# Kernel optimization log

Hardware: AMD Instinct MI355X
Metric: run time of the kernel (lower is better)

The kernel has to match this reference:

```python
import jax, jax.numpy as jnp
import numpy as np


def _ln(x, w, b, eps=1e-5):
    m = x.mean(-1, keepdims=True)
    v = jnp.mean((x - m) ** 2, axis=-1, keepdims=True)
    return (x - m) * jax.lax.rsqrt(v + eps) * w + b


def _to_seq(xc, g):
    # xc: [B,Di,H,W] -> [B,L,Di]; g0: row-major fwd, g1: row-major rev,
    # g2: col-major fwd, g3: col-major rev (CrossScan_1..4)
    if g >= 2:
        xc = xc.transpose(0, 1, 3, 2)
    s = xc.reshape(xc.shape[0], xc.shape[1], -1)
    if g % 2 == 1:
        s = jnp.flip(s, -1)
    return s.transpose(0, 2, 1)


def _from_seq(y, g, H, W):
    # y: [B,L,Di] -> [B,H,W,Di], inverse of _to_seq (CrossMerge_1..4)
    if g % 2 == 1:
        y = jnp.flip(y, 1)
    Bn, L, Di = y.shape
    if g >= 2:
        return y.reshape(Bn, W, H, Di).transpose(0, 2, 1, 3)
    return y.reshape(Bn, H, W, Di)


def _sscan(dA, dBx, Cm):
    # selective scan: h_t = dA_t*h + dBx_t ; y_t = <h_t, C_t>
    # dA,dBx: [B,L,Di,S], Cm: [B,L,S] -> y: [B,L,Di]
    def step(h, inp):
        a, bx, c = inp
        h = a * h + bx
        return h, jnp.einsum('bds,bs->bd', h, c)
    h0 = jnp.zeros(dA.shape[:1] + dA.shape[2:], dA.dtype)
    _, ys = jax.lax.scan(step, h0, (dA.transpose(1, 0, 2, 3), dBx.transpose(1, 0, 2, 3), Cm.transpose(1, 0, 2)))
    return ys.transpose(1, 0, 2)


def _ss2d(xc, g, H, W, ipw, ipb, cw, cb, xpw, dtw, dtb, A_log, Ds, onw, onb, opw, opb):
    R = dtw.shape[-1]
    S = A_log.shape[-1]
    xz = xc @ ipw.T + ipb                      # [B,H,W,2*Di]
    Di = xz.shape[-1] // 2
    xi, z = xz[..., :Di], xz[..., Di:]
    xi = xi.transpose(0, 3, 1, 2)              # [B,Di,H,W]
    xi = jax.lax.conv_general_dilated(xi, cw, (1, 1), [(1, 1), (1, 1)],
                                      dimension_numbers=('NCHW', 'OIHW', 'NCHW'),
                                      feature_group_count=Di) + cb[None, :, None, None]
    xi = jax.nn.silu(xi)
    seq = _to_seq(xi, g)                       # [B,L,Di]
    xdbl = seq @ xpw.T                         # [B,L,R+2S]
    dtr, Bm, Cm = xdbl[..., :R], xdbl[..., R:R + S], xdbl[..., R + S:]
    dt = jax.nn.softplus(dtr @ dtw.T + dtb)    # [B,L,Di]
    A = -jnp.exp(A_log)                        # [Di,S]
    dA = jnp.exp(dt[..., None] * A)            # [B,L,Di,S]
    dBx = (dt * seq)[..., None] * Bm[:, :, None, :]
    y = _sscan(dA, dBx, Cm) + Ds * seq
    y = _from_seq(y, g, H, W)                  # [B,H,W,Di]
    y = _ln(y, onw, onb)
    y = y * jax.nn.silu(z)
    return y @ opw.T + opb


def setup_inputs() -> dict:
    Bn, Hh, Ww, C = 8, 96, 96, 256
    Di = C // 4
    S = 1
    R = max(1, (Di + 15) // 16)
    key = jax.random.key(0)
    ks = jax.random.split(key, 12)
    nrm = lambda k, sh, s: jax.random.normal(k, sh, jnp.float32) * s
    return {
        'x': nrm(ks[0], (Bn, Hh * Ww, C), 1.0),
        'norm_w': jnp.ones((C,), jnp.float32), 'norm_b': jnp.zeros((C,), jnp.float32),
        'fc_w': nrm(ks[1], (C, C), 0.02), 'fc_b': jnp.zeros((C,), jnp.float32),
        'conv1d_w': nrm(ks[2], (1, 1, 3), 0.3),
        'in_proj_w': nrm(ks[3], (4, 2 * Di, Di), 0.05), 'in_proj_b': jnp.zeros((4, 2 * Di), jnp.float32),
        'conv2d_w': nrm(ks[4], (4, Di, 1, 3, 3), 0.2), 'conv2d_b': jnp.zeros((4, Di), jnp.float32),
        'x_proj_w': nrm(ks[5], (4, R + 2 * S, Di), 0.05),
        'dt_w': nrm(ks[6], (4, Di, R), 0.1), 'dt_b': nrm(ks[7], (4, Di), 0.1),
        'A_log': nrm(ks[8], (4, Di, S), 0.1),
        'Ds': jnp.ones((4, Di), jnp.float32),
        'out_norm_w': jnp.ones((4, Di), jnp.float32), 'out_norm_b': jnp.zeros((4, Di), jnp.float32),
        'out_proj_w': nrm(ks[9], (4, Di, Di), 0.05), 'out_proj_b': jnp.zeros((4, Di), jnp.float32),
        'proj_w': nrm(ks[10], (C, C), 0.02), 'proj_b': jnp.zeros((C,), jnp.float32),
        'skip_scale': jnp.ones((1,), jnp.float32),
        'H': Hh, 'W': Ww,
    }


def reference(x, norm_w, norm_b, fc_w, fc_b, conv1d_w, in_proj_w, in_proj_b, conv2d_w, conv2d_b,
              x_proj_w, dt_w, dt_b, A_log, Ds, out_norm_w, out_norm_b, out_proj_w, out_proj_b,
              proj_w, proj_b, skip_scale, H, W):
    B, N, C = x.shape
    xn = _ln(x, norm_w, norm_b)
    z_avg = xn.mean(1)                         # [B,C] (permute(0,2,1).mean(2))
    yg = jax.lax.conv_general_dilated(z_avg[:, None, :], conv1d_w, (1,), [(1, 1)],
                                      dimension_numbers=('NCH', 'OIH', 'NCH'))[:, 0, :]
    gate = jax.nn.sigmoid(z_avg @ fc_w.T + fc_b + yg)   # fc_out_2 [B,C]
    xg = xn.reshape(B, H, W, C)
    Dg = C // 4
    outs = [_ss2d(xg[..., g * Dg:(g + 1) * Dg], g, H, W,
                  in_proj_w[g], in_proj_b[g], conv2d_w[g], conv2d_b[g], x_proj_w[g],
                  dt_w[g], dt_b[g], A_log[g], Ds[g], out_norm_w[g], out_norm_b[g],
                  out_proj_w[g], out_proj_b[g]) for g in range(4)]
    xm = jnp.concatenate(outs, -1) * skip_scale * xg
    xm = xm.reshape(B, N, C) * gate[:, None, :]
    xm = _ln(xm, norm_w, norm_b)
    return xm @ proj_w.T + proj_b
```

## Files before the change

### kernel.cpp

```cpp
#include <hip/hip_runtime.h>
#include <math.h>

#define HH 96
#define WWI 96
#define NN 9216
#define CC 256
#define LL 9216
#define CHK 96
#define NCH 96
#define BB 8
#define BN (BB*NN)

__device__ __forceinline__ float softplusf(float x){
    float e = expf(-fabsf(x));
    return fmaxf(x, 0.f) + log1pf(e);
}
__device__ __forceinline__ float sigmf(float x){ return 1.f / (1.f + expf(-x)); }

__device__ __forceinline__ float wredsum(float v){
    #pragma unroll
    for(int o = 32; o > 0; o >>= 1) v += __shfl_xor(v, o, 64);
    return v;
}

__device__ __forceinline__ void wredsum2(float& s, float& q){
    #pragma unroll
    for(int o = 32; o > 0; o >>= 1){
        s += __shfl_xor(s, o, 64);
        q += __shfl_xor(q, o, 64);
    }
}

__device__ __forceinline__ void chunk_walk(int g, int chunk, int& base, int& step){
    if(g == 0){ base = chunk * 96;        step = 1;   }
    else if(g == 1){ base = 9215 - chunk * 96; step = -1; }
    else if(g == 2){ base = chunk;        step = 96;  }
    else { base = 9215 - chunk;           step = -96; }
}

__global__ __launch_bounds__(256) void k_stats(const float* __restrict__ x,
                                               float* __restrict__ mrs){
    int wid = threadIdx.x >> 6, lane = threadIdx.x & 63;
    size_t row = (size_t)blockIdx.x * 4 + wid;
    float4 v = ((const float4*)(x + row * CC))[lane];
    float s = wredsum(v.x + v.y + v.z + v.w);
    float q = wredsum(v.x*v.x + v.y*v.y + v.z*v.z + v.w*v.w);
    float m = s * (1.f/256.f);
    float var = q * (1.f/256.f) - m*m;
    float rs = rsqrtf(fmaxf(var, 0.f) + 1e-5f);
    if(lane == 0){ mrs[2*row] = m; mrs[2*row+1] = rs; }
}

__global__ __launch_bounds__(256) void k_stats2(const float* __restrict__ y,
                                                float* __restrict__ mrs2){
    int wid = threadIdx.x >> 6, lane = threadIdx.x & 63;
    size_t row = (size_t)blockIdx.x * 4 + wid;
    size_t b = row / NN, n = row - b * NN;
    int g = lane >> 4, c4 = (lane & 15) * 4;
    float4 v = *(const float4*)(y + (((size_t)b*4 + g)*NN + n)*64 + c4);
    float s = wredsum(v.x + v.y + v.z + v.w);
    float q = wredsum(v.x*v.x + v.y*v.y + v.z*v.z + v.w*v.w);
    float m = s * (1.f/256.f);
    float var = q * (1.f/256.f) - m*m;
    float rs = rsqrtf(fmaxf(var, 0.f) + 1e-5f);
    if(lane == 0){ mrs2[2*row] = m; mrs2[2*row+1] = rs; }
}

__global__ __launch_bounds__(256) void k_prew(const float* __restrict__ pw,
        const float* __restrict__ nw, const float* __restrict__ nb,
        const float* __restrict__ pb, float* __restrict__ Wn,
        float* __restrict__ wsum, float* __restrict__ cvec){
    int o = threadIdx.x;
    float ws = 0.f, cc = 0.f;
    for(int k = 0; k < 256; k++){
        float w = pw[(size_t)o * 256 + k];
        float wn = w * nw[k];
        Wn[(size_t)o * 256 + k] = wn;
        ws += wn; cc += w * nb[k];
    }
    wsum[o] = ws; cvec[o] = cc + pb[o];
}

__global__ __launch_bounds__(256) void k_zavg(const float* __restrict__ x,
        const float* __restrict__ mrs, const float* __restrict__ nw,
        const float* __restrict__ nb, float* __restrict__ zpart){
    int c = threadIdx.x, b = blockIdx.y, t0 = blockIdx.x * 256;
    float nwv = nw[c], nbv = nb[c];
    float s = 0.f;
    for(int i = 0; i < 256; i++){
        size_t r = (size_t)b * NN + t0 + i;
        s += (x[r * CC + c] - mrs[2*r]) * mrs[2*r+1] * nwv + nbv;
    }
    zpart[((size_t)b * 36 + blockIdx.x) * CC + c] = s;
}

__global__ __launch_bounds__(256) void k_gate(const float* __restrict__ zpart,
        const float* __restrict__ fcw, const float* __restrict__ fcb,
        const float* __restrict__ w1d, float* __restrict__ gate){
    __shared__ float za[CC];
    int c = threadIdx.x, b = blockIdx.x;
    float s = 0.f;
    for(int t = 0; t < 36; t++) s += zpart[((size_t)b * 36 + t) * CC + c];
    za[c] = s * (1.f/(float)NN);
    __syncthreads();
    float zm1 = (c > 0)     ? za[c-1] : 0.f;
    float zp1 = (c < CC-1)  ? za[c+1] : 0.f;
    float acc = fcb[c] + w1d[0]*zm1 + w1d[1]*za[c] + w1d[2]*zp1;
    const float* wr = fcw + (size_t)c * CC;
    for(int k = 0; k < CC; k++) acc += za[k] * wr[k];
    gate[b * CC + c] = sigmf(acc);
}

template<int ZPRE>
__global__ __launch_bounds__(256) void k_ipconv(const float* __restrict__ x,
        const float* __restrict__ mrs, const float* __restrict__ nw,
        const float* __restrict__ nb, const float* __restrict__ ipw,
        const float* __restrict__ ipb, const float* __restrict__ cw,
        const float* __restrict__ cb, float* __restrict__ out,
        float* __restrict__ zbuf){
    int tile = blockIdx.x, b = blockIdx.y, g = blockIdx.z;
    int h0 = (tile / 12) * 8, w0 = (tile % 12) * 8;
    __shared__ float xs[100 * 64];
    __shared__ float xi[100 * 64];
    int tid = threadIdx.x;
    for(int i = tid; i < 6400; i += 256){
        int p = i >> 6, k = i & 63;
        int ph = h0 + p / 10 - 1, pw = w0 + p % 10 - 1;
        float v = 0.f;
        if(ph >= 0 && ph < HH && pw >= 0 && pw < WWI){
            size_t r = (size_t)b * NN + ph * WWI + pw;
            v = (x[r * CC + g*64 + k] - mrs[2*r]) * mrs[2*r+1]
                * nw[g*64 + k] + nb[g*64 + k];
        }
        xs[i] = v;
    }
    __syncthreads();
    int c = tid & 63, q = tid >> 6;
    {
        float wv[64];
        const float* wr = ipw + ((size_t)(g * 128 + c)) * 64;
        #pragma unroll
        for(int k = 0; k < 64; k++) wv[k] = wr[k];
        float bias = ipb[g * 128 + c];
        for(int p = q * 25; p < q * 25 + 25; p++){
            int ph = h0 + p / 10 - 1, pw = w0 + p % 10 - 1;
            bool valid = (ph >= 0 && ph < HH && pw >= 0 && pw < WWI);
            float acc = bias;
            const float* xp = &xs[p * 64];
            #pragma unroll
            for(int k = 0; k < 64; k++) acc += xp[k] * wv[k];
            xi[p * 64 + c] = valid ? acc : 0.f;
        }
    }
    __syncthreads();
    float wk[9];
    const float* wp = cw + ((size_t)(g * 64 + c)) * 9;
    #pragma unroll
    for(int j = 0; j < 9; j++) wk[j] = wp[j];
    float bias2 = cb[g * 64 + c];
    for(int pi = q * 16; pi < q * 16 + 16; pi++){
        int py = pi >> 3, px = pi & 7;
        float acc = bias2;
        #pragma unroll
        for(int dy = 0; dy < 3; dy++)
            #pragma unroll
            for(int dx = 0; dx < 3; dx++)
                acc += xi[((py + dy) * 10 + px + dx) * 64 + c] * wk[dy*3 + dx];
        float sv = acc * sigmf(acc);
        size_t r = (size_t)b * NN + (h0 + py) * WWI + (w0 + px);
        out[r * CC + g*64 + c] = sv;
    }
    if(ZPRE){
        float wzv[64];
        const float* wr = ipw + ((size_t)(g * 128 + 64 + c)) * 64;
        #pragma unroll
        for(int k = 0; k < 64; k++) wzv[k] = wr[k];
        float zbv = ipb[g * 128 + 64 + c];
        size_t zb0 = ((size_t)(b * 4 + g)) * NN;
        for(int p16 = 0; p16 < 16; p16++){
            int p = q * 16 + p16;
            int py = p >> 3, px = p & 7;
            const float* xp = &xs[((py + 1) * 10 + (px + 1)) * 64];
            float acc = zbv;
            #pragma unroll
            for(int k = 0; k < 64; k++) acc += xp[k] * wzv[k];
            zbuf[(zb0 + (size_t)((h0 + py) * WWI + (w0 + px))) * 64 + c]
                = acc * sigmf(acc);
        }
    }
}

__global__ __launch_bounds__(64) void k_scan1(const float* __restrict__ out,
        const float* __restrict__ xpw, const float* __restrict__ dtw,
        const float* __restrict__ dtb, const float* __restrict__ alog,
        float* __restrict__ ap_out, float* __restrict__ h_out){
    int chunk = blockIdx.x, gb = blockIdx.y;
    int g = gb >> 3, b = gb & 7, d = threadIdx.x;
    __shared__ float s_seq[CHK * 65];
    __shared__ float s_xd[CHK * 6];
    __shared__ float s_w[6 * 64];
    int base, step; chunk_walk(g, chunk, base, step);
    const float* xg = out + (size_t)b * NN * CC + g * 64;
    for(int j = 0; j < CHK; j++)
        s_seq[j * 65 + d] = xg[(size_t)(base + j * step) * CC + d];
    for(int i = d; i < 384; i += 64) s_w[i] = xpw[g * 384 + i];
    __syncthreads();
    for(int idx = d; idx < CHK*6; idx += 64){
        int l = idx / 6, j = idx % 6;
        float acc = 0.f;
        const float* sr = &s_seq[l * 65];
        const float* wr = &s_w[j * 64];
        #pragma unroll
        for(int k = 0; k < 64; k++) acc += sr[k] * wr[k];
        s_xd[idx] = acc;
    }
    __syncthreads();
    int gd = g * 64 + d;
    float Av = -expf(alog[gd]);
    float db = dtb[gd];
    float w0 = dtw[gd*4], w1 = dtw[gd*4+1], w2 = dtw[gd*4+2], w3 = dtw[gd*4+3];
    float h = 0.f, apd = 1.f;
    #pragma unroll 4
    for(int l = 0; l < CHK; l++){
        const float* xd = &s_xd[l * 6];
        float xv = s_seq[l*65 + d];
        float dt = softplusf(xd[0]*w0 + xd[1]*w1 + xd[2]*w2 + xd[3]*w3 + db);
        float a = expf(dt * Av);
        h = a*h + dt*xv*xd[4];
        apd *= a;
    }
    int ob = (gb * NCH + chunk) * 64 + d;
    ap_out[ob] = apd; h_out[ob] = h;
}

__global__ __launch_bounds__(256) void k_scan2(const float* __restrict__ ap,
        const float* __restrict__ he, float* __restrict__ hinit){
    int idx = blockIdx.x * 256 + threadIdx.x;
    int gb = idx >> 6, d = idx & 63;
    float h = 0.f;
    for(int c = 0; c < NCH; c++){
        int o = (gb * NCH + c) * 64 + d;
        hinit[o] = h;
        h = ap[o]*h + he[o];
    }
}

template<int ZPRE>
__global__ __launch_bounds__(64) void k_scan3(float* __restrict__ out,
        const float* __restrict__ x, const float* __restrict__ mrs,
        const float* __restrict__ nw, const float* __restrict__ nb,
        const float* __restrict__ ipw, const float* __restrict__ ipb,
        const float* __restrict__ xpw, const float* __restrict__ dtw,
        const float* __restrict__ dtb, const float* __restrict__ alog,
        const float* __restrict__ Dsp, const float* __restrict__ onw,
        const float* __restrict__ onb, const float* __restrict__ hinit,
        const float* __restrict__ zbuf){
    int chunk = blockIdx.x, gb = blockIdx.y;
    int g = gb >> 3, b = gb & 7, d = threadIdx.x;
    __shared__ float s_seq[CHK * 65];
    __shared__ float s_xd[CHK * 6];
    __shared__ float s_w[6 * 64];
    __shared__ float xnt[(ZPRE ? 1 : CHK) * 65];
    int base, step; chunk_walk(g, chunk, base, step);
    float* xg = out + (size_t)b * NN * CC + g * 64;
    for(int j = 0; j < CHK; j++)
        s_seq[j * 65 + d] = xg[(size_t)(base + j * step) * CC + d];
    if(!ZPRE){
        float nwv = nw[g*64 + d], nbv = nb[g*64 + d];
        for(int j = 0; j < CHK; j++){
            int n = base + j * step;
            size_t r = (size_t)b * NN + n;
            xnt[j * 65 + d] = (x[r * CC + g*64 + d] - mrs[2*r]) * mrs[2*r+1] * nwv + nbv;
        }
    }
    for(int i = d; i < 384; i += 64) s_w[i] = xpw[g * 384 + i];
    __syncthreads();
    for(int idx = d; idx < CHK*6; idx += 64){
        int l = idx / 6, j = idx % 6;
        float acc = 0.f;
        const float* sr = &s_seq[l * 65];
        const float* wr = &s_w[j * 64];
        #pragma unroll
        for(int k = 0; k < 64; k++) acc += sr[k] * wr[k];
        s_xd[idx] = acc;
    }
    __syncthreads();
    int gd = g * 64 + d;
    float Av = -expf(alog[gd]);
    float db = dtb[gd];
    float Dv = Dsp[gd];
    float w0 = dtw[gd*4], w1 = dtw[gd*4+1], w2 = dtw[gd*4+2], w3 = dtw[gd*4+3];
    float h = hinit[(gb * NCH + chunk) * 64 + d];
    #pragma unroll 4
    for(int l = 0; l < CHK; l++){
        const float* xd = &s_xd[l * 6];
        float xv = s_seq[l*65 + d];
        float dt = softplusf(xd[0]*w0 + xd[1]*w1 + xd[2]*w2 + xd[3]*w3 + db);
        float a = expf(dt * Av);
        h = a*h + dt*xv*xd[4];
        s_seq[l*65 + d] = h * xd[5] + Dv * xv;
    }
    float wON = onw[gd], bON = onb[gd];
    float wz[ZPRE ? 1 : 64];
    float zb = 0.f;
    if(!ZPRE){
        const float* wr = ipw + ((size_t)(g * 128 + 64 + d)) * 64;
        #pragma unroll
        for(int k = 0; k < 64; k++) wz[k] = wr[k];
        zb = ipb[g * 128 + 64 + d];
    }
    const float* zp = zbuf + (((size_t)(b * 4 + g)) * NN) * 64 + d;
    #pragma unroll 4
    for(int l = 0; l < CHK; l++){
        float y = s_seq[l*65 + d];
        float s = y, q = y * y;
        wredsum2(s, q);
        float m = s * (1.f/64.f);
        float var = q * (1.f/64.f) - m*m;
        float rs = rsqrtf(fmaxf(var, 0.f) + 1e-5f);
        float lny = (y - m) * rs * wON + bON;
        int n = base + l * step;
        float zs;
        if(ZPRE){
            zs = zp[(size_t)n * 64];
        } else {
            float z = zb;
            const float* xp = &xnt[l * 65];
            #pragma unroll
            for(int k = 0; k < 64; k++) z += xp[k] * wz[k];
            zs = z * sigmf(z);
        }
        xg[(size_t)n * CC + d] = lny * zs;
    }
}

template<int TOZ>
__global__ __launch_bounds__(64) void k_out2(float* __restrict__ out,
        const float* __restrict__ x, const float* __restrict__ mrs,
        const float* __restrict__ nw, const float* __restrict__ nb,
        const float* __restrict__ opw, const float* __restrict__ opb,
        const float* __restrict__ gate, const float* __restrict__ skip,
        float* __restrict__ zo){
    int tile = blockIdx.x, b = blockIdx.y, g = blockIdx.z;
    int n0 = tile * 64, t = threadIdx.x;
    __shared__ float ly[64 * 65];
    __shared__ float xnt[64 * 65];
    float* xg = out + (size_t)b * NN * CC + g * 64;
    float nwv = nw[g*64 + t], nbv = nb[g*64 + t];
    for(int p = 0; p < 64; p++){
        size_t r = (size_t)b * NN + n0 + p;
        ly[p * 65 + t] = xg[(size_t)(n0 + p) * CC + t];
        xnt[p * 65 + t] = (x[r * CC + g*64 + t] - mrs[2*r]) * mrs[2*r+1] * nwv + nbv;
    }
    __syncthreads();
    float wv[64];
    const float* wr = opw + ((size_t)(g * 64 + t)) * 64;
    #pragma unroll
    for(int k = 0; k < 64; k++) wv[k] = wr[k];
    float bias = opb[g * 64 + t];
    float gv = gate[b * CC + g*64 + t];
    float sk = skip[0];
    for(int p = 0; p < 64; p++){
        float acc = bias;
        const float* yp = &ly[p * 65];
        #pragma unroll
        for(int k = 0; k < 64; k++) acc += yp[k] * wv[k];
        float res = acc * sk * xnt[p * 65 + t] * gv;
        if(TOZ)
            zo[((size_t)(b*4 + g)*NN + n0 + p)*64 + t] = res;
        else
            xg[(size_t)(n0 + p) * CC + t] = res;
    }
}

__global__ __launch_bounds__(256) void k_final(float* __restrict__ out,
        const float* __restrict__ nw, const float* __restrict__ nb,
        const float* __restrict__ pw, const float* __restrict__ pb){
    __shared__ float A[16 * 256];
    __shared__ float ps[256], pq[256];
    __shared__ float mrow[16], rrow[16];
    int n0 = blockIdx.x * 16;
    for(int i = threadIdx.x; i < 4096; i += 256)
        A[i] = out[(size_t)n0 * CC + i];
    __syncthreads();
    {
        int r = threadIdx.x >> 4, t16 = threadIdx.x & 15;
        float s = 0.f, q = 0.f;
        for(int j = 0; j < 16; j++){
            float v = A[r*256 + t16*16 + j];
            s += v; q += v*v;
        }
        ps[threadIdx.x] = s; pq[threadIdx.x] = q;
    }
    __syncthreads();
    if(threadIdx.x < 16){
        float ss = 0.f, qq = 0.f;
        for(int j = 0; j < 16; j++){ ss += ps[threadIdx.x*16 + j]; qq += pq[threadIdx.x*16 + j]; }
        float m = ss * (1.f/256.f);
        float var = qq * (1.f/256.f) - m*m;
        mrow[threadIdx.x] = m;
        rrow[threadIdx.x] = rsqrtf(fmaxf(var, 0.f) + 1e-5f);
    }
    __syncthreads();
    for(int i = threadIdx.x; i < 4096; i += 256){
        int r = i >> 8, c = i & 255;
        A[i] = (A[i] - mrow[r]) * rrow[r] * nw[c] + nb[c];
    }
    __syncthreads();
    int o = threadIdx.x;
    float acc[16];
    #pragma unroll
    for(int p = 0; p < 16; p++) acc[p] = 0.f;
    for(int kt = 0; kt < 4; kt++){
        float wv[64];
        const float4* wr = (const float4*)(pw + (size_t)o * CC + kt * 64);
        #pragma unroll
        for(int j = 0; j < 16; j++){
            float4 tq = wr[j];
            wv[4*j+0] = tq.x; wv[4*j+1] = tq.y;
            wv[4*j+2] = tq.z; wv[4*j+3] = tq.w;
        }
        #pragma unroll
        for(int p = 0; p < 16; p++){
            const float* ar = &A[p*256 + kt*64];
            float a = 0.f;
            #pragma unroll
            for(int k = 0; k < 64; k++) a += ar[k] * wv[k];
            acc[p] += a;
        }
    }
    float pbv = pb[o];
    #pragma unroll
    for(int p = 0; p < 16; p++)
        out[(size_t)(n0 + p) * CC + o] = acc[p] + pbv;
}

__global__ __launch_bounds__(256) void k_final2(const float* __restrict__ y,
        const float* __restrict__ mrs2, const float* __restrict__ Wn,
        const float* __restrict__ wsum, const float* __restrict__ cvec,
        float* __restrict__ out){
    int o = threadIdx.x;
    int r0 = blockIdx.x * 16;
    int b  = r0 / NN;
    int n0 = r0 - b * NN;
    float acc[16];
    #pragma unroll
    for(int r = 0; r < 16; r++) acc[r] = 0.f;
    for(int kt = 0; kt < 4; kt++){
        float wv[64];
        const float4* wr = (const float4*)(Wn + (size_t)o * 256 + kt * 64);
        #pragma unroll
        for(int j = 0; j < 16; j++){
            float4 t4 = wr[j];
            wv[4*j+0] = t4.x; wv[4*j+1] = t4.y;
            wv[4*j+2] = t4.z; wv[4*j+3] = t4.w;
        }
        const float* ab = y + ((size_t)(b*4 + kt)*NN + n0) * 64;
        #pragma unroll 4
        for(int r = 0; r < 16; r++){
            const float* ar = ab + (size_t)r * 64;
            float s0 = 0.f, s1 = 0.f;
            #pragma unroll
            for(int j = 0; j < 32; j++){
                s0 += ar[j]      * wv[j];
                s1 += ar[j + 32] * wv[j + 32];
            }
            acc[r] += s0 + s1;
        }
    }
    float wso = wsum[o], co = cvec[o];
    #pragma unroll
    for(int r = 0; r < 16; r++){
        float m  = mrs2[2*(size_t)(r0 + r)];
        float rs = mrs2[2*(size_t)(r0 + r) + 1];
        out[(size_t)(r0 + r) * CC + o] = rs * acc[r] - m * rs * wso + co;
    }
}

extern "C" void kernel_launch(void* const* d_in, const int* in_sizes, int n_in,
                              void* d_out, int out_size, void* d_ws, size_t ws_size,
                              hipStream_t stream){
    const float* x    = (const float*)d_in[0];
    const float* nw   = (const float*)d_in[1];
    const float* nb   = (const float*)d_in[2];
    const float* fcw  = (const float*)d_in[3];
    const float* fcb  = (const float*)d_in[4];
    const float* w1d  = (const float*)d_in[5];
    const float* ipw  = (const float*)d_in[6];
    const float* ipb  = (const float*)d_in[7];
    const float* cw   = (const float*)d_in[8];
    const float* cb   = (const float*)d_in[9];
    const float* xpw  = (const float*)d_in[10];
    const float* dtw  = (const float*)d_in[11];
    const float* dtb  = (const float*)d_in[12];
    const float* alog = (const float*)d_in[13];
    const float* Dsp  = (const float*)d_in[14];
    const float* onw  = (const float*)d_in[15];
    const float* onb  = (const float*)d_in[16];
    const float* opw  = (const float*)d_in[17];
    const float* opb  = (const float*)d_in[18];
    const float* pw   = (const float*)d_in[19];
    const float* pb   = (const float*)d_in[20];
    const float* skip = (const float*)d_in[21];

    char* base = (char*)d_ws;
    float* mrs  = (float*)base;
    float* gate = (float*)(base +  589824ull);
    float* ap   = (float*)(base +  598016ull);
    float* he   = (float*)(base + 1384448ull);
    float* hi   = (float*)(base + 2170880ull);
    float* zbuf = (float*)(base + 2957312ull);
    float* mrs2 = (float*)(base + 78454784ull);
    float* Wn   = (float*)(base + 79044608ull);
    float* wsum = (float*)(base + 79306752ull);
    float* cvec = (float*)(base + 79307776ull);
    float* zpart = ap;
    float* out  = (float*)d_out;
    (void)in_sizes; (void)n_in; (void)out_size;

    const size_t T1 = 78454784ull;
    const size_t T2 = 79308800ull;
    bool usez = ws_size >= T1;
    bool usef2 = ws_size >= T2;

    if(usef2)
        k_prew<<<1, 256, 0, stream>>>(pw, nw, nb, pb, Wn, wsum, cvec);
    k_stats <<<18432, 256, 0, stream>>>(x, mrs);
    k_zavg  <<<dim3(36, 8), 256, 0, stream>>>(x, mrs, nw, nb, zpart);
    k_gate  <<<8, 256, 0, stream>>>(zpart, fcw, fcb, w1d, gate);
    if(usez){
        k_ipconv<1><<<dim3(144, 8, 4), 256, 0, stream>>>(x, mrs, nw, nb, ipw, ipb,
                                                         cw, cb, out, zbuf);
    } else {
        k_ipconv<0><<<dim3(144, 8, 4), 256, 0, stream>>>(x, mrs, nw, nb, ipw, ipb,
                                                         cw, cb, out, zbuf);
    }
    k_scan1 <<<dim3(96, 32), 64, 0, stream>>>(out, xpw, dtw, dtb, alog, ap, he);
    k_scan2 <<<8, 256, 0, stream>>>(ap, he, hi);
    if(usez){
        k_scan3<1><<<dim3(96, 32), 64, 0, stream>>>(out, x, mrs, nw, nb, ipw, ipb,
                                                    xpw, dtw, dtb, alog, Dsp, onw,
                                                    onb, hi, zbuf);
    } else {
        k_scan3<0><<<dim3(96, 32), 64, 0, stream>>>(out, x, mrs, nw, nb, ipw, ipb,
                                                    xpw, dtw, dtb, alog, Dsp, onw,
                                                    onb, hi, zbuf);
    }
    if(usef2){
        k_out2<1><<<dim3(144, 8, 4), 64, 0, stream>>>(out, x, mrs, nw, nb, opw, opb,
                                                      gate, skip, zbuf);
        k_stats2<<<18432, 256, 0, stream>>>(zbuf, mrs2);
        k_final2<<<4608, 256, 0, stream>>>(zbuf, mrs2, Wn, wsum, cvec, out);
    } else {
        k_out2<0><<<dim3(144, 8, 4), 64, 0, stream>>>(out, x, mrs, nw, nb, opw, opb,
                                                      gate, skip, zbuf);
        k_final <<<4608, 256, 0, stream>>>(out, nw, nb, pw, pb);
    }
}
```

Before: 1.341 ms.

## Split fused in-projection and depthwise conv into separate kernels with intermediate buffer

Replaces the fused k_ipconv kernel, which recomputed the in-projection on haloed 10x10 tiles, with two kernels. k_inproj does LayerNorm plus the in-projection on 128-pixel strips and writes xi to a new workspace buffer and SiLU(z) to zbuf. k_conv then runs the 3x3 depthwise conv plus SiLU from that buffer. This removes the redundant halo matmul work and the large shared-memory footprint, at the cost of an extra global round trip for xi. The new path is only taken when the workspace is large enough.

```diff
diff --git a/kernel.cpp b/kernel.cpp
--- a/kernel.cpp
+++ b/kernel.cpp
@@ -109,6 +109,99 @@
     const float* wr = fcw + (size_t)c * CC;
     for(int k = 0; k < CC; k++) acc += za[k] * wr[k];
     gate[b * CC + c] = sigmf(acc);
+}
+
+__global__ __launch_bounds__(256) void k_inproj(const float* __restrict__ x,
+        const float* __restrict__ mrs, const float* __restrict__ nw,
+        const float* __restrict__ nb, const float* __restrict__ ipw,
+        const float* __restrict__ ipb, float* __restrict__ xib,
+        float* __restrict__ zbuf){
+    int tile = blockIdx.x, b = blockIdx.y, g = blockIdx.z;
+    int n0 = tile * 128;
+    __shared__ float xs[128 * 64];
+    int tid = threadIdx.x;
+    for(int idx = tid; idx < 2048; idx += 256){
+        int p = idx >> 4, k4 = (idx & 15) * 4;
+        size_t r = (size_t)b * NN + n0 + p;
+        float4 v = *(const float4*)(x + r * CC + g*64 + k4);
+        float m = mrs[2*r], rs = mrs[2*r+1];
+        float4 w4 = *(const float4*)(nw + g*64 + k4);
+        float4 b4 = *(const float4*)(nb + g*64 + k4);
+        float4 o;
+        o.x = (v.x - m)*rs*w4.x + b4.x;
+        o.y = (v.y - m)*rs*w4.y + b4.y;
+        o.z = (v.z - m)*rs*w4.z + b4.z;
+        o.w = (v.w - m)*rs*w4.w + b4.w;
+        *(float4*)(xs + p*64 + k4) = o;
+    }
+    __syncthreads();
+    int c = tid & 63, ph = tid >> 6;
+    float wx[64], wz[64];
+    {
+        const float* wrx = ipw + ((size_t)(g*128 + c)) * 64;
+        const float* wrz = ipw + ((size_t)(g*128 + 64 + c)) * 64;
+        #pragma unroll
+        for(int k = 0; k < 64; k++){ wx[k] = wrx[k]; wz[k] = wrz[k]; }
+    }
+    float bx = ipb[g*128 + c], bz = ipb[g*128 + 64 + c];
+    size_t obase = ((size_t)(b*4 + g)) * NN + n0;
+    for(int p = ph*32; p < ph*32 + 32; p++){
+        const float4* xp = (const float4*)(xs + p*64);
+        float a0 = 0.f, a1 = 0.f, z0 = 0.f, z1 = 0.f;
+        #pragma unroll
+        for(int k4 = 0; k4 < 16; k4 += 2){
+            float4 u = xp[k4], v = xp[k4+1];
+            a0 += u.x*wx[4*k4+0]; a1 += u.y*wx[4*k4+1];
+            a0 += u.z*wx[4*k4+2]; a1 += u.w*wx[4*k4+3];
+            z0 += u.x*wz[4*k4+0]; z1 += u.y*wz[4*k4+1];
+            z0 += u.z*wz[4*k4+2]; z1 += u.w*wz[4*k4+3];
+            a0 += v.x*wx[4*k4+4]; a1 += v.y*wx[4*k4+5];
+            a0 += v.z*wx[4*k4+6]; a1 += v.w*wx[4*k4+7];
+            z0 += v.x*wz[4*k4+4]; z1 += v.y*wz[4*k4+5];
+            z0 += v.z*wz[4*k4+6]; z1 += v.w*wz[4*k4+7];
+        }
+        float xv = bx + a0 + a1;
+        float zv = bz + z0 + z1;
+        xib[(obase + p)*64 + c] = xv;
+        zbuf[(obase + p)*64 + c] = zv * sigmf(zv);
+    }
+}
+
+__global__ __launch_bounds__(256) void k_conv(const float* __restrict__ xib,
+        const float* __restrict__ cw, const float* __restrict__ cb,
+        float* __restrict__ out){
+    int tile = blockIdx.x, b = blockIdx.y, g = blockIdx.z;
+    int h0 = (tile/12)*8, w0 = (tile%12)*8;
+    __shared__ float xs[100*64];
+    int tid = threadIdx.x;
+    size_t ibase = ((size_t)(b*4+g)) * NN;
+    for(int i = tid; i < 6400; i += 256){
+        int p = i >> 6, k = i & 63;
+        int ph = h0 + p/10 - 1, pw = w0 + p%10 - 1;
+        float v = 0.f;
+        if(ph >= 0 && ph < HH && pw >= 0 && pw < WWI)
+            v = xib[(ibase + (size_t)(ph*WWI + pw))*64 + k];
+        xs[i] = v;
+    }
+    __syncthreads();
+    int c = tid & 63, q = tid >> 6;
+    float wk[9];
+    const float* wp = cw + ((size_t)(g*64 + c))*9;
+    #pragma unroll
+    for(int j = 0; j < 9; j++) wk[j] = wp[j];
+    float bias2 = cb[g*64 + c];
+    for(int pi = q*16; pi < q*16+16; pi++){
+        int py = pi >> 3, px = pi & 7;
+        float acc = bias2;
+        #pragma unroll
+        for(int dy = 0; dy < 3; dy++)
+            #pragma unroll
+            for(int dx = 0; dx < 3; dx++)
+                acc += xs[((py+dy)*10 + px+dx)*64 + c] * wk[dy*3+dx];
+        float sv = acc * sigmf(acc);
+        size_t r = (size_t)b*NN + (h0+py)*WWI + (w0+px);
+        out[r*CC + g*64 + c] = sv;
+    }
 }
 
 template<int ZPRE>
@@ -514,21 +607,28 @@
     float* Wn   = (float*)(base + 79044608ull);
     float* wsum = (float*)(base + 79306752ull);
     float* cvec = (float*)(base + 79307776ull);
+    float* xib  = (float*)(base + 79308800ull);
     float* zpart = ap;
     float* out  = (float*)d_out;
     (void)in_sizes; (void)n_in; (void)out_size;
 
     const size_t T1 = 78454784ull;
     const size_t T2 = 79308800ull;
-    bool usez = ws_size >= T1;
-    bool usef2 = ws_size >= T2;
+    const size_t T3 = 154806272ull;
+    bool usez    = ws_size >= T1;
+    bool usef2   = ws_size >= T2;
+    bool usesplit= ws_size >= T3;
 
     if(usef2)
         k_prew<<<1, 256, 0, stream>>>(pw, nw, nb, pb, Wn, wsum, cvec);
     k_stats <<<18432, 256, 0, stream>>>(x, mrs);
     k_zavg  <<<dim3(36, 8), 256, 0, stream>>>(x, mrs, nw, nb, zpart);
     k_gate  <<<8, 256, 0, stream>>>(zpart, fcw, fcb, w1d, gate);
-    if(usez){
+    if(usesplit){
+        k_inproj<<<dim3(72, 8, 4), 256, 0, stream>>>(x, mrs, nw, nb, ipw, ipb,
+                                                     xib, zbuf);
+        k_conv  <<<dim3(144, 8, 4), 256, 0, stream>>>(xib, cw, cb, out);
+    } else if(usez){
         k_ipconv<1><<<dim3(144, 8, 4), 256, 0, stream>>>(x, mrs, nw, nb, ipw, ipb,
                                                          cw, cb, out, zbuf);
     } else {
```

After: 1.332 ms. Within noise of the previous version (-0.7%).
